# Performance work log

Measured on AMD Instinct MI355X. Metric: run time of the kernel, lower is better.

The kernel has to match this reference:

```python
import jax, jax.numpy as jnp
import numpy as np

# Static configuration (mirrors init_kwargs)
F_REAL = 64
F_CAT = 32
OUT = 32
HID = [64, 64, 32]
IDX_REAL_MISS = np.arange(16)   # indices into the real-feature subset
IDX_CAT_MISS = np.arange(8)     # indices into the cat-feature subset
N_CAT_MISS = len(IDX_CAT_MISS)
B = 8192


def wn(v, g):
    """PyTorch weight_norm: w = g * v / ||v|| with norm over input dim (last axis).
    v: [F, out, in], g: [F, out] -> w: [F, out, in]"""
    return g[..., None] * v / jnp.linalg.norm(v, axis=-1, keepdims=True)


def setup_inputs() -> dict:
    key = jax.random.key(0)
    ks = jax.random.split(key, 16)
    s = 0.3
    values = jax.random.normal(ks[0], (B, 96), dtype=jnp.float32)
    miss = (jax.random.uniform(ks[1], (B, 96)) < 0.1).astype(jnp.float32)
    tabular = jnp.stack([values, miss], axis=1)  # [B, 2, 96]
    # Per-feature weight-normed MLP params, stacked over F_REAL features.
    inp = {
        "tabular": tabular,
        "v0": jax.random.normal(ks[2], (F_REAL, HID[0], 1)) * s,
        "g0": jnp.ones((F_REAL, HID[0])),
        "b0": jax.random.normal(ks[3], (F_REAL, HID[0])) * 0.01,
        "v1": jax.random.normal(ks[4], (F_REAL, HID[1], HID[0])) * s,
        "g1": jnp.ones((F_REAL, HID[1])),
        "b1": jax.random.normal(ks[5], (F_REAL, HID[1])) * 0.01,
        "v2": jax.random.normal(ks[6], (F_REAL, HID[2], HID[1])) * s,
        "g2": jnp.ones((F_REAL, HID[2])),
        "b2": jax.random.normal(ks[7], (F_REAL, HID[2])) * 0.01,
        "v3": jax.random.normal(ks[8], (F_REAL, OUT, HID[2])) * s,
        "g3": jnp.ones((F_REAL, OUT)),
        "cat_linear": jax.random.normal(ks[9], (F_CAT, OUT)) * s,
        "missing_emb": jax.random.normal(ks[10], (len(IDX_REAL_MISS) + N_CAT_MISS, OUT)) * s,
        "bias": jnp.zeros((1, OUT)),
    }
    return inp


def reference(tabular, v0, g0, b0, v1, g1, b1, v2, g2, b2, v3, g3,
              cat_linear, missing_emb, bias):
    # Eval mode: nn.Dropout / nn.Dropout1d are identity.
    values, is_missing = tabular[:, 0], tabular[:, 1]
    val_real, miss_real = values[:, :F_REAL], is_missing[:, :F_REAL]
    val_cat, miss_cat = values[:, F_REAL:F_REAL + F_CAT], is_missing[:, F_REAL:F_REAL + F_CAT]

    # Batched tiny MLPs over all real features at once.
    w0 = wn(v0, g0)[:, :, 0]                  # [F, H0] (scalar input)
    h = jax.nn.relu(val_real[:, :, None] * w0[None] + b0[None])        # [B,F,H0]
    h = jax.nn.relu(jnp.einsum('bfi,foi->bfo', h, wn(v1, g1)) + b1[None])  # [B,F,H1]
    h = jax.nn.relu(jnp.einsum('bfi,foi->bfo', h, wn(v2, g2)) + b2[None])  # [B,F,H2]
    feat_real = jnp.einsum('bfi,foi->bfo', h, wn(v3, g3))               # [B,F,OUT]

    feat_cat = cat_linear[None] * val_cat[:, :, None]                   # [B,Fc,OUT]

    feat_real = feat_real * (1.0 - miss_real[:, :, None])
    feat_cat = feat_cat * (1.0 - miss_cat[:, :, None])

    # Scatter-fill missing embeddings (add is exact since masked entries are zero)
    feat_real = feat_real.at[:, IDX_REAL_MISS, :].add(
        missing_emb[N_CAT_MISS:][None] * miss_real[:, IDX_REAL_MISS, None])
    feat_cat = feat_cat.at[:, IDX_CAT_MISS, :].add(
        missing_emb[:N_CAT_MISS][None] * miss_cat[:, IDX_CAT_MISS, None])

    features = jnp.concatenate([feat_real, feat_cat], axis=1)           # [B,96,OUT]
    logits = jnp.sum(features, axis=1) + bias                           # [B,OUT]
    return (logits, features)
```

## Files before the change

### kernel.cpp

```cpp
#include <hip/hip_runtime.h>
#include <math.h>

typedef _Float16 f16;
typedef _Float16 f16x8 __attribute__((ext_vector_type(8)));
typedef float f32x4 __attribute__((ext_vector_type(4)));

#define NB 8192
#define LOGN (NB * 32)

#define OFF_W0   0
#define OFF_SC1  16384
#define OFF_SC2  32768
#define OFF_SC3  40960
#define OFF_B1   49152
#define OFF_B2   573440
#define OFF_B3   835584

__global__ __launch_bounds__(256)
void prep_norm(const float* __restrict__ v0, const float* __restrict__ g0,
               const float* __restrict__ v1, const float* __restrict__ g1,
               const float* __restrict__ v2, const float* __restrict__ g2,
               const float* __restrict__ v3, const float* __restrict__ g3,
               float* __restrict__ ws) {
    int t = blockIdx.x * blockDim.x + threadIdx.x;
    if (t < 4096) {
        float v = v0[t];
        ws[OFF_W0 / 4 + t] = g0[t] * (v >= 0.f ? 1.f : -1.f);
    } else if (t < 8192) {
        int r = t - 4096;
        const float* vp = v1 + (size_t)r * 64;
        float ss = 0.f;
        #pragma unroll
        for (int i = 0; i < 16; ++i) {
            float4 x = *(const float4*)(vp + i * 4);
            ss += x.x * x.x + x.y * x.y + x.z * x.z + x.w * x.w;
        }
        ws[OFF_SC1 / 4 + r] = g1[r] * __frsqrt_rn(ss);
    } else if (t < 10240) {
        int r = t - 8192;
        const float* vp = v2 + (size_t)r * 64;
        float ss = 0.f;
        #pragma unroll
        for (int i = 0; i < 16; ++i) {
            float4 x = *(const float4*)(vp + i * 4);
            ss += x.x * x.x + x.y * x.y + x.z * x.z + x.w * x.w;
        }
        ws[OFF_SC2 / 4 + r] = g2[r] * __frsqrt_rn(ss);
    } else if (t < 12288) {
        int r = t - 10240;
        const float* vp = v3 + (size_t)r * 32;
        float ss = 0.f;
        #pragma unroll
        for (int i = 0; i < 8; ++i) {
            float4 x = *(const float4*)(vp + i * 4);
            ss += x.x * x.x + x.y * x.y + x.z * x.z + x.w * x.w;
        }
        ws[OFF_SC3 / 4 + r] = g3[r] * __frsqrt_rn(ss);
    }
}

__global__ __launch_bounds__(256)
void prep_frag(const float* __restrict__ v1, const float* __restrict__ v2,
               const float* __restrict__ v3, const float* __restrict__ ws,
               f16* __restrict__ b1f, f16* __restrict__ b2f, f16* __restrict__ b3f) {
    int t = blockIdx.x * blockDim.x + threadIdx.x;
    if (t < 262144) {
        int i = t & 7, lane = (t >> 3) & 63, nt = (t >> 9) & 3, ks = (t >> 11) & 1, f = t >> 12;
        int k = ks * 32 + ((lane >> 4) << 3) + i;
        int n = nt * 16 + (lane & 15);
        int r = f * 64 + n;
        b1f[t] = (f16)(v1[(size_t)r * 64 + k] * ws[OFF_SC1 / 4 + r]);
    } else if (t < 393216) {
        int t2 = t - 262144;
        int i = t2 & 7, lane = (t2 >> 3) & 63, nt = (t2 >> 9) & 1, ks = (t2 >> 10) & 1, f = t2 >> 11;
        int k = ks * 32 + ((lane >> 4) << 3) + i;
        int n = nt * 16 + (lane & 15);
        int r = f * 32 + n;
        b2f[t2] = (f16)(v2[(size_t)r * 64 + k] * ws[OFF_SC2 / 4 + r]);
    } else {
        int t3 = t - 393216;
        int i = t3 & 7, lane = (t3 >> 3) & 63, nt = (t3 >> 9) & 1, f = t3 >> 10;
        int k = ((lane >> 4) << 3) + i;
        int n = nt * 16 + (lane & 15);
        int r = f * 32 + n;
        b3f[t3] = (f16)(v3[(size_t)r * 32 + k] * ws[OFF_SC3 / 4 + r]);
    }
}

__global__ __launch_bounds__(256, 2)
void nam_fused(const float* __restrict__ tab, const float* __restrict__ w0,
               const f16* __restrict__ b1f, const f16* __restrict__ b2f,
               const f16* __restrict__ b3f,
               const float* __restrict__ b0, const float* __restrict__ b1,
               const float* __restrict__ b2, const float* __restrict__ memb,
               const float* __restrict__ cat_linear, const float* __restrict__ bias,
               float* __restrict__ feat, float* __restrict__ logits) {
    __shared__ char lds[4][8192];
    __shared__ f16 tv[32][98];
    __shared__ f16 tm[32][98];
    __shared__ float lsum[32][36];

    const int wave = threadIdx.x >> 6, lane = threadIdx.x & 63;
    const int lq = lane >> 4, lr = lane & 15;
    const int rowbase = blockIdx.x * 32;
    const int f0 = wave * 16;
    char* h1b = lds[wave];
    char* h2b = lds[wave] + 4096;

    for (int i = threadIdx.x; i < 32 * 36; i += 256)
        (&lsum[0][0])[i] = 0.f;

    #pragma unroll
    for (int it = 0; it < 6; ++it) {
        int g = it * 256 + threadIdx.x;
        int row = g / 48, q = g - row * 48;
        float4 x = *(const float4*)(tab + (size_t)(rowbase + row) * 192 + q * 4);
        int c = q * 4;
        if (c < 96) {
            tv[row][c + 0] = (f16)x.x; tv[row][c + 1] = (f16)x.y;
            tv[row][c + 2] = (f16)x.z; tv[row][c + 3] = (f16)x.w;
        } else {
            int cm = c - 96;
            tm[row][cm + 0] = (f16)x.x; tm[row][cm + 1] = (f16)x.y;
            tm[row][cm + 2] = (f16)x.z; tm[row][cm + 3] = (f16)x.w;
        }
    }
    __syncthreads();

    float lacc[2][2][4];
    #pragma unroll
    for (int mt = 0; mt < 2; ++mt)
        #pragma unroll
        for (int nt = 0; nt < 2; ++nt)
            #pragma unroll
            for (int j = 0; j < 4; ++j) lacc[mt][nt][j] = 0.f;

    #pragma unroll 1
    for (int fi = 0; fi < 16; ++fi) {
        const int f = f0 + fi;

        f16x8 B1[2][4], B2[2][2], B3[2];
        {
            const f16* p1 = b1f + f * 4096 + lane * 8;
            #pragma unroll
            for (int ks = 0; ks < 2; ++ks)
                #pragma unroll
                for (int nt = 0; nt < 4; ++nt)
                    B1[ks][nt] = *(const f16x8*)(p1 + ks * 2048 + nt * 512);
            const f16* p2 = b2f + f * 2048 + lane * 8;
            #pragma unroll
            for (int ks = 0; ks < 2; ++ks)
                #pragma unroll
                for (int nt = 0; nt < 2; ++nt)
                    B2[ks][nt] = *(const f16x8*)(p2 + ks * 1024 + nt * 512);
            const f16* p3 = b3f + f * 1024 + lane * 8;
            #pragma unroll
            for (int nt = 0; nt < 2; ++nt)
                B3[nt] = *(const f16x8*)(p3 + nt * 512);
        }

        float b1v[4], b2v[2];
        #pragma unroll
        for (int nt = 0; nt < 4; ++nt) b1v[nt] = b1[f * 64 + nt * 16 + lr];
        #pragma unroll
        for (int nt = 0; nt < 2; ++nt) b2v[nt] = b2[f * 32 + nt * 16 + lr];
        float vmt[2], msr[2];
        #pragma unroll
        for (int mt = 0; mt < 2; ++mt) {
            vmt[mt] = (float)tv[mt * 16 + lr][f];
            msr[mt] = (float)tm[mt * 16 + lr][f];
        }

        f16x8 A0[2][2];
        #pragma unroll
        for (int ks = 0; ks < 2; ++ks) {
            float w0v[8], b0v[8];
            *(float4*)&w0v[0] = *(const float4*)(w0 + f * 64 + ks * 32 + lq * 8);
            *(float4*)&w0v[4] = *(const float4*)(w0 + f * 64 + ks * 32 + lq * 8 + 4);
            *(float4*)&b0v[0] = *(const float4*)(b0 + f * 64 + ks * 32 + lq * 8);
            *(float4*)&b0v[4] = *(const float4*)(b0 + f * 64 + ks * 32 + lq * 8 + 4);
            #pragma unroll
            for (int mt = 0; mt < 2; ++mt)
                #pragma unroll
                for (int i = 0; i < 8; ++i)
                    A0[mt][ks][i] = (f16)fmaxf(fmaf(vmt[mt], w0v[i], b0v[i]), 0.f);
        }

        f32x4 acc1[2][4];
        #pragma unroll
        for (int mt = 0; mt < 2; ++mt)
            #pragma unroll
            for (int nt = 0; nt < 4; ++nt) acc1[mt][nt] = (f32x4){0.f, 0.f, 0.f, 0.f};
        #pragma unroll
        for (int ks = 0; ks < 2; ++ks)
            #pragma unroll
            for (int nt = 0; nt < 4; ++nt)
                #pragma unroll
                for (int mt = 0; mt < 2; ++mt)
                    acc1[mt][nt] = __builtin_amdgcn_mfma_f32_16x16x32_f16(A0[mt][ks], B1[ks][nt], acc1[mt][nt], 0, 0, 0);
        #pragma unroll
        for (int mt = 0; mt < 2; ++mt)
            #pragma unroll
            for (int nt = 0; nt < 4; ++nt) {
                int n = nt * 16 + lr;
                int colb = ((n >> 3) << 4) + ((n & 7) << 1);
                #pragma unroll
                for (int j = 0; j < 4; ++j) {
                    int row = mt * 16 + lq * 4 + j;
                    int byte = ((row << 7) + colb) ^ ((row & 7) << 4);
                    *(f16*)(h1b + byte) = (f16)fmaxf(acc1[mt][nt][j] + b1v[nt], 0.f);
                }
            }

        f16x8 A1[2][2];
        #pragma unroll
        for (int mt = 0; mt < 2; ++mt)
            #pragma unroll
            for (int ks = 0; ks < 2; ++ks) {
                int row = mt * 16 + lr;
                int byte = ((row << 7) + ((ks * 4 + lq) << 4)) ^ ((row & 7) << 4);
                A1[mt][ks] = *(const f16x8*)(h1b + byte);
            }
        f32x4 acc2[2][2];
        #pragma unroll
        for (int mt = 0; mt < 2; ++mt)
            #pragma unroll
            for (int nt = 0; nt < 2; ++nt) acc2[mt][nt] = (f32x4){0.f, 0.f, 0.f, 0.f};
        #pragma unroll
        for (int ks = 0; ks < 2; ++ks)
            #pragma unroll
            for (int nt = 0; nt < 2; ++nt)
                #pragma unroll
                for (int mt = 0; mt < 2; ++mt)
                    acc2[mt][nt] = __builtin_amdgcn_mfma_f32_16x16x32_f16(A1[mt][ks], B2[ks][nt], acc2[mt][nt], 0, 0, 0);
        #pragma unroll
        for (int mt = 0; mt < 2; ++mt)
            #pragma unroll
            for (int nt = 0; nt < 2; ++nt) {
                int n = nt * 16 + lr;
                int colb = ((n >> 3) << 4) + ((n & 7) << 1);
                #pragma unroll
                for (int j = 0; j < 4; ++j) {
                    int row = mt * 16 + lq * 4 + j;
                    int byte = ((row << 7) + colb) ^ ((row & 7) << 4);
                    *(f16*)(h2b + byte) = (f16)fmaxf(acc2[mt][nt][j] + b2v[nt], 0.f);
                }
            }

        f16x8 A2[2];
        #pragma unroll
        for (int mt = 0; mt < 2; ++mt) {
            int row = mt * 16 + lr;
            int byte = ((row << 7) + (lq << 4)) ^ ((row & 7) << 4);
            A2[mt] = *(const f16x8*)(h2b + byte);
        }
        f32x4 accT[2][2];
        #pragma unroll
        for (int nt = 0; nt < 2; ++nt)
            #pragma unroll
            for (int mt = 0; mt < 2; ++mt) accT[nt][mt] = (f32x4){0.f, 0.f, 0.f, 0.f};
        #pragma unroll
        for (int nt = 0; nt < 2; ++nt)
            #pragma unroll
            for (int mt = 0; mt < 2; ++mt)
                accT[nt][mt] = __builtin_amdgcn_mfma_f32_16x16x32_f16(B3[nt], A2[mt], accT[nt][mt], 0, 0, 0);

        const bool hasemb = (f < 16);
        float4 e[2] = {{0, 0, 0, 0}, {0, 0, 0, 0}};
        if (hasemb) {
            #pragma unroll
            for (int nt = 0; nt < 2; ++nt)
                e[nt] = *(const float4*)(memb + (8 + f) * 32 + nt * 16 + lq * 4);
        }
        #pragma unroll
        for (int mt = 0; mt < 2; ++mt) {
            const int row = rowbase + mt * 16 + lr;
            const float m = msr[mt];
            const float keep = 1.f - m;
            float* dst = feat + (size_t)row * 3072 + f * 32 + lq * 4;
            #pragma unroll
            for (int nt = 0; nt < 2; ++nt) {
                float4 v;
                v.x = accT[nt][mt][0] * keep;
                v.y = accT[nt][mt][1] * keep;
                v.z = accT[nt][mt][2] * keep;
                v.w = accT[nt][mt][3] * keep;
                if (hasemb) {
                    v.x = fmaf(e[nt].x, m, v.x);
                    v.y = fmaf(e[nt].y, m, v.y);
                    v.z = fmaf(e[nt].z, m, v.z);
                    v.w = fmaf(e[nt].w, m, v.w);
                }
                *(float4*)(dst + nt * 16) = v;
                lacc[mt][nt][0] += v.x;
                lacc[mt][nt][1] += v.y;
                lacc[mt][nt][2] += v.z;
                lacc[mt][nt][3] += v.w;
            }
        }
    }

    #pragma unroll
    for (int mt = 0; mt < 2; ++mt)
        #pragma unroll
        for (int nt = 0; nt < 2; ++nt)
            #pragma unroll
            for (int j = 0; j < 4; ++j)
                atomicAdd(&lsum[mt * 16 + lr][nt * 16 + lq * 4 + j], lacc[mt][nt][j]);
    __syncthreads();

    {
        const int row = threadIdx.x >> 3;
        const int o4 = (threadIdx.x & 7) * 4;
        const int grow = rowbase + row;
        float4 s = *(const float4*)(bias + o4);
        s.x += lsum[row][o4 + 0];
        s.y += lsum[row][o4 + 1];
        s.z += lsum[row][o4 + 2];
        s.w += lsum[row][o4 + 3];
        float* fb = feat + (size_t)grow * 3072 + 64 * 32 + o4;
        #pragma unroll
        for (int fc = 0; fc < 32; ++fc) {
            float val = (float)tv[row][64 + fc];
            float m   = (float)tm[row][64 + fc];
            float vk = val * (1.f - m);
            float4 cl4 = *(const float4*)(cat_linear + fc * 32 + o4);
            float4 r;
            r.x = cl4.x * vk; r.y = cl4.y * vk; r.z = cl4.z * vk; r.w = cl4.w * vk;
            if (fc < 8) {
                float4 mb4 = *(const float4*)(memb + fc * 32 + o4);
                r.x = fmaf(mb4.x, m, r.x);
                r.y = fmaf(mb4.y, m, r.y);
                r.z = fmaf(mb4.z, m, r.z);
                r.w = fmaf(mb4.w, m, r.w);
            }
            *(float4*)(fb + fc * 32) = r;
            s.x += r.x; s.y += r.y; s.z += r.z; s.w += r.w;
        }
        *(float4*)(logits + (size_t)grow * 32 + o4) = s;
    }
}

extern "C" void kernel_launch(void* const* d_in, const int* in_sizes, int n_in,
                              void* d_out, int out_size, void* d_ws, size_t ws_size,
                              hipStream_t stream) {
    const float* tab        = (const float*)d_in[0];
    const float* v0         = (const float*)d_in[1];
    const float* g0         = (const float*)d_in[2];
    const float* b0         = (const float*)d_in[3];
    const float* v1         = (const float*)d_in[4];
    const float* g1         = (const float*)d_in[5];
    const float* b1         = (const float*)d_in[6];
    const float* v2         = (const float*)d_in[7];
    const float* g2         = (const float*)d_in[8];
    const float* b2         = (const float*)d_in[9];
    const float* v3         = (const float*)d_in[10];
    const float* g3         = (const float*)d_in[11];
    const float* cat_linear = (const float*)d_in[12];
    const float* memb       = (const float*)d_in[13];
    const float* bias       = (const float*)d_in[14];

    float* out    = (float*)d_out;
    float* logits = out;
    float* feat   = out + LOGN;

    float* ws   = (float*)d_ws;
    float* w0   = (float*)((char*)d_ws + OFF_W0);
    f16*   b1f  = (f16*)((char*)d_ws + OFF_B1);
    f16*   b2f  = (f16*)((char*)d_ws + OFF_B2);
    f16*   b3f  = (f16*)((char*)d_ws + OFF_B3);

    prep_norm<<<48, 256, 0, stream>>>(v0, g0, v1, g1, v2, g2, v3, g3, ws);
    prep_frag<<<1792, 256, 0, stream>>>(v1, v2, v3, ws, b1f, b2f, b3f);

    nam_fused<<<256, 256, 0, stream>>>(tab, w0, b1f, b2f, b3f, b0, b1, b2,
                                       memb, cat_linear, bias, feat, logits);
}
```

Before: 58.93 us.

## Split work into 16-row blocks of 8 waves with 8 features each

The fused kernel now runs 512 blocks of 512 threads, each covering 16 rows with 8 waves handling 8 real features apiece, instead of 256 blocks of 4 waves covering 32 rows and 16 features. LDS scratch per wave shrinks and the h2 swizzle is adjusted to the smaller tile. The goal is to fill more of the GPU's compute units and raise occupancy for a memory-bound write of features. In exchange, each wave reloads its B fragments for half as many rows, so weight fragment traffic per row doubles. The categorical epilogue also moves from float4 to scalar stores.

```diff
diff --git a/kernel.cpp b/kernel.cpp
--- a/kernel.cpp
+++ b/kernel.cpp
@@ -87,7 +87,7 @@
     }
 }
 
-__global__ __launch_bounds__(256, 2)
+__global__ __launch_bounds__(512, 4)
 void nam_fused(const float* __restrict__ tab, const float* __restrict__ w0,
                const f16* __restrict__ b1f, const f16* __restrict__ b2f,
                const f16* __restrict__ b3f,
@@ -95,24 +95,23 @@
                const float* __restrict__ b2, const float* __restrict__ memb,
                const float* __restrict__ cat_linear, const float* __restrict__ bias,
                float* __restrict__ feat, float* __restrict__ logits) {
-    __shared__ char lds[4][8192];
-    __shared__ f16 tv[32][98];
-    __shared__ f16 tm[32][98];
-    __shared__ float lsum[32][36];
+    __shared__ char h1s[8][2048];
+    __shared__ char h2s[8][1024];
+    __shared__ f16 tv[16][98];
+    __shared__ f16 tm[16][98];
+    __shared__ float lsum[16][33];
 
     const int wave = threadIdx.x >> 6, lane = threadIdx.x & 63;
     const int lq = lane >> 4, lr = lane & 15;
-    const int rowbase = blockIdx.x * 32;
-    const int f0 = wave * 16;
-    char* h1b = lds[wave];
-    char* h2b = lds[wave] + 4096;
-
-    for (int i = threadIdx.x; i < 32 * 36; i += 256)
+    const int rowbase = blockIdx.x * 16;
+    const int f0 = wave * 8;
+    char* h1b = h1s[wave];
+    char* h2b = h2s[wave];
+
+    for (int i = threadIdx.x; i < 16 * 33; i += 512)
         (&lsum[0][0])[i] = 0.f;
 
-    #pragma unroll
-    for (int it = 0; it < 6; ++it) {
-        int g = it * 256 + threadIdx.x;
+    for (int g = threadIdx.x; g < 768; g += 512) {
         int row = g / 48, q = g - row * 48;
         float4 x = *(const float4*)(tab + (size_t)(rowbase + row) * 192 + q * 4);
         int c = q * 4;
@@ -127,16 +126,14 @@
     }
     __syncthreads();
 
-    float lacc[2][2][4];
+    float lacc[2][4];
     #pragma unroll
-    for (int mt = 0; mt < 2; ++mt)
-        #pragma unroll
-        for (int nt = 0; nt < 2; ++nt)
-            #pragma unroll
-            for (int j = 0; j < 4; ++j) lacc[mt][nt][j] = 0.f;
+    for (int nt = 0; nt < 2; ++nt)
+        #pragma unroll
+        for (int j = 0; j < 4; ++j) lacc[nt][j] = 0.f;
 
     #pragma unroll 1
-    for (int fi = 0; fi < 16; ++fi) {
+    for (int fi = 0; fi < 8; ++fi) {
         const int f = f0 + fi;
 
         f16x8 B1[2][4], B2[2][2], B3[2];
@@ -164,14 +161,10 @@
         for (int nt = 0; nt < 4; ++nt) b1v[nt] = b1[f * 64 + nt * 16 + lr];
         #pragma unroll
         for (int nt = 0; nt < 2; ++nt) b2v[nt] = b2[f * 32 + nt * 16 + lr];
-        float vmt[2], msr[2];
-        #pragma unroll
-        for (int mt = 0; mt < 2; ++mt) {
-            vmt[mt] = (float)tv[mt * 16 + lr][f];
-            msr[mt] = (float)tm[mt * 16 + lr][f];
-        }
-
-        f16x8 A0[2][2];
+        const float vmt = (float)tv[lr][f];
+        const float msr = (float)tm[lr][f];
+
+        f16x8 A0[2];
         #pragma unroll
         for (int ks = 0; ks < 2; ++ks) {
             float w0v[8], b0v[8];
@@ -180,90 +173,67 @@
             *(float4*)&b0v[0] = *(const float4*)(b0 + f * 64 + ks * 32 + lq * 8);
             *(float4*)&b0v[4] = *(const float4*)(b0 + f * 64 + ks * 32 + lq * 8 + 4);
             #pragma unroll
-            for (int mt = 0; mt < 2; ++mt)
-                #pragma unroll
-                for (int i = 0; i < 8; ++i)
-                    A0[mt][ks][i] = (f16)fmaxf(fmaf(vmt[mt], w0v[i], b0v[i]), 0.f);
-        }
-
-        f32x4 acc1[2][4];
-        #pragma unroll
-        for (int mt = 0; mt < 2; ++mt)
-            #pragma unroll
-            for (int nt = 0; nt < 4; ++nt) acc1[mt][nt] = (f32x4){0.f, 0.f, 0.f, 0.f};
+            for (int i = 0; i < 8; ++i)
+                A0[ks][i] = (f16)fmaxf(fmaf(vmt, w0v[i], b0v[i]), 0.f);
+        }
+
+        f32x4 acc1[4];
+        #pragma unroll
+        for (int nt = 0; nt < 4; ++nt) acc1[nt] = (f32x4){0.f, 0.f, 0.f, 0.f};
         #pragma unroll
         for (int ks = 0; ks < 2; ++ks)
             #pragma unroll
             for (int nt = 0; nt < 4; ++nt)
-                #pragma unroll
-                for (int mt = 0; mt < 2; ++mt)
-                    acc1[mt][nt] = __builtin_amdgcn_mfma_f32_16x16x32_f16(A0[mt][ks], B1[ks][nt], acc1[mt][nt], 0, 0, 0);
-        #pragma unroll
-        for (int mt = 0; mt < 2; ++mt)
-            #pragma unroll
-            for (int nt = 0; nt < 4; ++nt) {
-                int n = nt * 16 + lr;
-                int colb = ((n >> 3) << 4) + ((n & 7) << 1);
-                #pragma unroll
-                for (int j = 0; j < 4; ++j) {
-                    int row = mt * 16 + lq * 4 + j;
-                    int byte = ((row << 7) + colb) ^ ((row & 7) << 4);
-                    *(f16*)(h1b + byte) = (f16)fmaxf(acc1[mt][nt][j] + b1v[nt], 0.f);
-                }
+                acc1[nt] = __builtin_amdgcn_mfma_f32_16x16x32_f16(A0[ks], B1[ks][nt], acc1[nt], 0, 0, 0);
+        #pragma unroll
+        for (int nt = 0; nt < 4; ++nt) {
+            int n = nt * 16 + lr;
+            int colb = ((n >> 3) << 4) + ((n & 7) << 1);
+            #pragma unroll
+            for (int j = 0; j < 4; ++j) {
+                int row = lq * 4 + j;
+                int byte = ((row << 7) + colb) ^ ((row & 7) << 4);
+                *(f16*)(h1b + byte) = (f16)fmaxf(acc1[nt][j] + b1v[nt], 0.f);
             }
-
-        f16x8 A1[2][2];
-        #pragma unroll
-        for (int mt = 0; mt < 2; ++mt)
-            #pragma unroll
-            for (int ks = 0; ks < 2; ++ks) {
-                int row = mt * 16 + lr;
-                int byte = ((row << 7) + ((ks * 4 + lq) << 4)) ^ ((row & 7) << 4);
-                A1[mt][ks] = *(const f16x8*)(h1b + byte);
+        }
+
+        f16x8 A1[2];
+        #pragma unroll
+        for (int ks = 0; ks < 2; ++ks) {
+            int byte = ((lr << 7) + ((ks * 4 + lq) << 4)) ^ ((lr & 7) << 4);
+            A1[ks] = *(const f16x8*)(h1b + byte);
+        }
+        f32x4 acc2[2];
+        #pragma unroll
+        for (int nt = 0; nt < 2; ++nt) acc2[nt] = (f32x4){0.f, 0.f, 0.f, 0.f};
+        #pragma unroll
+        for (int ks = 0; ks < 2; ++ks)
+            #pragma unroll
+            for (int nt = 0; nt < 2; ++nt)
+                acc2[nt] = __builtin_amdgcn_mfma_f32_16x16x32_f16(A1[ks], B2[ks][nt], acc2[nt], 0, 0, 0);
+        #pragma unroll
+        for (int nt = 0; nt < 2; ++nt) {
+            int n = nt * 16 + lr;
+            int colb = ((n >> 3) << 4) + ((n & 7) << 1);
+            #pragma unroll
+            for (int j = 0; j < 4; ++j) {
+                int row = lq * 4 + j;
+                int byte = ((row << 6) + colb) ^ ((row & 3) << 4);
+                *(f16*)(h2b + byte) = (f16)fmaxf(acc2[nt][j] + b2v[nt], 0.f);
             }
-        f32x4 acc2[2][2];
-        #pragma unroll
-        for (int mt = 0; mt < 2; ++mt)
-            #pragma unroll
-            for (int nt = 0; nt < 2; ++nt) acc2[mt][nt] = (f32x4){0.f, 0.f, 0.f, 0.f};
-        #pragma unroll
-        for (int ks = 0; ks < 2; ++ks)
-            #pragma unroll
-            for (int nt = 0; nt < 2; ++nt)
-                #pragma unroll
-                for (int mt = 0; mt < 2; ++mt)
-                    acc2[mt][nt] = __builtin_amdgcn_mfma_f32_16x16x32_f16(A1[mt][ks], B2[ks][nt], acc2[mt][nt], 0, 0, 0);
-        #pragma unroll
-        for (int mt = 0; mt < 2; ++mt)
-            #pragma unroll
-            for (int nt = 0; nt < 2; ++nt) {
-                int n = nt * 16 + lr;
-                int colb = ((n >> 3) << 4) + ((n & 7) << 1);
-                #pragma unroll
-                for (int j = 0; j < 4; ++j) {
-                    int row = mt * 16 + lq * 4 + j;
-                    int byte = ((row << 7) + colb) ^ ((row & 7) << 4);
-                    *(f16*)(h2b + byte) = (f16)fmaxf(acc2[mt][nt][j] + b2v[nt], 0.f);
-                }
-            }
-
-        f16x8 A2[2];
-        #pragma unroll
-        for (int mt = 0; mt < 2; ++mt) {
-            int row = mt * 16 + lr;
-            int byte = ((row << 7) + (lq << 4)) ^ ((row & 7) << 4);
-            A2[mt] = *(const f16x8*)(h2b + byte);
-        }
-        f32x4 accT[2][2];
+        }
+
+        f16x8 A2;
+        {
+            int byte = ((lr << 6) + (lq << 4)) ^ ((lr & 3) << 4);
+            A2 = *(const f16x8*)(h2b + byte);
+        }
+        f32x4 accT[2];
+        #pragma unroll
+        for (int nt = 0; nt < 2; ++nt) accT[nt] = (f32x4){0.f, 0.f, 0.f, 0.f};
         #pragma unroll
         for (int nt = 0; nt < 2; ++nt)
-            #pragma unroll
-            for (int mt = 0; mt < 2; ++mt) accT[nt][mt] = (f32x4){0.f, 0.f, 0.f, 0.f};
-        #pragma unroll
-        for (int nt = 0; nt < 2; ++nt)
-            #pragma unroll
-            for (int mt = 0; mt < 2; ++mt)
-                accT[nt][mt] = __builtin_amdgcn_mfma_f32_16x16x32_f16(B3[nt], A2[mt], accT[nt][mt], 0, 0, 0);
+            accT[nt] = __builtin_amdgcn_mfma_f32_16x16x32_f16(B3[nt], A2, accT[nt], 0, 0, 0);
 
         const bool hasemb = (f < 16);
         float4 e[2] = {{0, 0, 0, 0}, {0, 0, 0, 0}};
@@ -272,19 +242,18 @@
             for (int nt = 0; nt < 2; ++nt)
                 e[nt] = *(const float4*)(memb + (8 + f) * 32 + nt * 16 + lq * 4);
         }
-        #pragma unroll
-        for (int mt = 0; mt < 2; ++mt) {
-            const int row = rowbase + mt * 16 + lr;
-            const float m = msr[mt];
+        {
+            const int row = rowbase + lr;
+            const float m = msr;
             const float keep = 1.f - m;
             float* dst = feat + (size_t)row * 3072 + f * 32 + lq * 4;
             #pragma unroll
             for (int nt = 0; nt < 2; ++nt) {
                 float4 v;
-                v.x = accT[nt][mt][0] * keep;
-                v.y = accT[nt][mt][1] * keep;
-                v.z = accT[nt][mt][2] * keep;
-                v.w = accT[nt][mt][3] * keep;
+                v.x = accT[nt][0] * keep;
+                v.y = accT[nt][1] * keep;
+                v.z = accT[nt][2] * keep;
+                v.w = accT[nt][3] * keep;
                 if (hasemb) {
                     v.x = fmaf(e[nt].x, m, v.x);
                     v.y = fmaf(e[nt].y, m, v.y);
@@ -292,52 +261,37 @@
                     v.w = fmaf(e[nt].w, m, v.w);
                 }
                 *(float4*)(dst + nt * 16) = v;
-                lacc[mt][nt][0] += v.x;
-                lacc[mt][nt][1] += v.y;
-                lacc[mt][nt][2] += v.z;
-                lacc[mt][nt][3] += v.w;
+                lacc[nt][0] += v.x;
+                lacc[nt][1] += v.y;
+                lacc[nt][2] += v.z;
+                lacc[nt][3] += v.w;
             }
         }
     }
 
     #pragma unroll
-    for (int mt = 0; mt < 2; ++mt)
-        #pragma unroll
-        for (int nt = 0; nt < 2; ++nt)
-            #pragma unroll
-            for (int j = 0; j < 4; ++j)
-                atomicAdd(&lsum[mt * 16 + lr][nt * 16 + lq * 4 + j], lacc[mt][nt][j]);
+    for (int nt = 0; nt < 2; ++nt)
+        #pragma unroll
+        for (int j = 0; j < 4; ++j)
+            atomicAdd(&lsum[lr][nt * 16 + lq * 4 + j], lacc[nt][j]);
     __syncthreads();
 
     {
-        const int row = threadIdx.x >> 3;
-        const int o4 = (threadIdx.x & 7) * 4;
+        const int row = threadIdx.x >> 5;
+        const int o = threadIdx.x & 31;
         const int grow = rowbase + row;
-        float4 s = *(const float4*)(bias + o4);
-        s.x += lsum[row][o4 + 0];
-        s.y += lsum[row][o4 + 1];
-        s.z += lsum[row][o4 + 2];
-        s.w += lsum[row][o4 + 3];
-        float* fb = feat + (size_t)grow * 3072 + 64 * 32 + o4;
+        float s = bias[o] + lsum[row][o];
+        float* fb = feat + (size_t)grow * 3072 + 64 * 32 + o;
         #pragma unroll
         for (int fc = 0; fc < 32; ++fc) {
             float val = (float)tv[row][64 + fc];
             float m   = (float)tm[row][64 + fc];
-            float vk = val * (1.f - m);
-            float4 cl4 = *(const float4*)(cat_linear + fc * 32 + o4);
-            float4 r;
-            r.x = cl4.x * vk; r.y = cl4.y * vk; r.z = cl4.z * vk; r.w = cl4.w * vk;
-            if (fc < 8) {
-                float4 mb4 = *(const float4*)(memb + fc * 32 + o4);
-                r.x = fmaf(mb4.x, m, r.x);
-                r.y = fmaf(mb4.y, m, r.y);
-                r.z = fmaf(mb4.z, m, r.z);
-                r.w = fmaf(mb4.w, m, r.w);
-            }
-            *(float4*)(fb + fc * 32) = r;
-            s.x += r.x; s.y += r.y; s.z += r.z; s.w += r.w;
-        }
-        *(float4*)(logits + (size_t)grow * 32 + o4) = s;
+            float r = cat_linear[fc * 32 + o] * val * (1.f - m);
+            if (fc < 8) r = fmaf(memb[fc * 32 + o], m, r);
+            fb[fc * 32] = r;
+            s += r;
+        }
+        logits[(size_t)grow * 32 + o] = s;
     }
 }
 
@@ -373,6 +327,6 @@
     prep_norm<<<48, 256, 0, stream>>>(v0, g0, v1, g1, v2, g2, v3, g3, ws);
     prep_frag<<<1792, 256, 0, stream>>>(v1, v2, v3, ws, b1f, b2f, b3f);
 
-    nam_fused<<<256, 256, 0, stream>>>(tab, w0, b1f, b2f, b3f, b0, b1, b2,
+    nam_fused<<<512, 512, 0, stream>>>(tab, w0, b1f, b2f, b3f, b0, b1, b2,
                                        memb, cat_linear, bias, feat, logits);
 }
```

After: 59.59 us. Within noise of the previous version (+1.1%).
